# Kernel optimization log

Measured on AMD Instinct MI355X. Metric: run time of the kernel, lower is better.

## Reference

```python
import jax, jax.numpy as jnp
import numpy as np

N, E = 40000, 640000
IN_DIM, EDGE_DIM, HID = 128, 64, 128


def setup_inputs() -> dict:
    key = jax.random.key(0)
    ks = jax.random.split(key, 10)
    x = jax.random.normal(ks[0], (N, IN_DIM), dtype=jnp.float32)
    edge_index = jax.random.randint(ks[1], (2, E), 0, N, dtype=jnp.int64)
    edge_attr = jax.random.normal(ks[2], (E, EDGE_DIM), dtype=jnp.float32)
    # learned params (xavier-ish scaling)
    Wh_w = jax.random.normal(ks[3], (EDGE_DIM, HID), dtype=jnp.float32) / np.sqrt(EDGE_DIM)
    Wh_b = jnp.zeros((HID,), dtype=jnp.float32)
    Wn_w = jax.random.normal(ks[4], (2 * IN_DIM, HID), dtype=jnp.float32) / np.sqrt(2 * IN_DIM)
    Wn_b = jnp.zeros((HID,), dtype=jnp.float32)
    w_e = jax.random.normal(ks[5], (HID, 1), dtype=jnp.float32) / np.sqrt(HID)
    ft_w = jax.random.normal(ks[6], (IN_DIM, IN_DIM), dtype=jnp.float32) / np.sqrt(IN_DIM)
    ft_b = jnp.zeros((IN_DIM,), dtype=jnp.float32)
    return {"x": x, "edge_index": edge_index, "edge_attr": edge_attr,
            "Wh_w": Wh_w, "Wh_b": Wh_b, "Wn_w": Wn_w, "Wn_b": Wn_b,
            "w_e": w_e, "ft_w": ft_w, "ft_b": ft_b}


def reference(x, edge_index, edge_attr, Wh_w, Wh_b, Wn_w, Wn_b, w_e, ft_w, ft_b):
    src, dst = edge_index[0], edge_index[1]
    # gather endpoint features and run edge MLP: relu(W_h(e) + W_n([x_src; x_dst]))
    node_feat = jnp.concatenate([x[src], x[dst]], axis=1)          # [E, 2*in_dim]
    edge_h = edge_attr @ Wh_w + Wh_b                               # [E, hid]
    node_h = node_feat @ Wn_w + Wn_b                               # [E, hid]
    combined = jax.nn.relu(edge_h + node_h)
    scores = (combined @ w_e)[:, 0]                                # [E]
    alpha = jax.nn.softmax(scores, axis=0)                         # softmax over all edges
    # scatter-add weighted dst features into src nodes (same-type branch)
    local = jnp.zeros_like(x).at[src].add(-alpha[:, None] * x[dst])
    out = x + local
    out = out + out @ ft_w + ft_b
    return out
```

## Files before the change

kernel.cpp:

```cpp
#include <hip/hip_runtime.h>
#include <math.h>

#define N_NODES 40000
#define E_EDGES 640000
#define IN_DIM 128
#define EDGE_DIM 64
#define HID 128
#define EB 10000
#define NPART (EB * 4)

typedef unsigned int u32;
typedef unsigned short u16;
typedef __attribute__((ext_vector_type(4))) float f32x4;
typedef __attribute__((ext_vector_type(8))) short bf16x8;

__device__ __forceinline__ float bf_lo(u32 d) { return __uint_as_float(d << 16); }
__device__ __forceinline__ float bf_hi(u32 d) { return __uint_as_float(d & 0xffff0000u); }
__device__ __forceinline__ u16 f2bf(float f) {
    u32 u = __float_as_uint(f);
    return (u16)((u + 0x7fffu + ((u >> 16) & 1u)) >> 16);
}
__device__ __forceinline__ u32 pack_bf(float lo, float hi) {
    return ((u32)f2bf(hi) << 16) | (u32)f2bf(lo);
}


__global__ __launch_bounds__(256) void k_init(const float* __restrict__ x,
                                              u16* __restrict__ xb,
                                              u32* __restrict__ counts) {
    int i = blockIdx.x * 256 + threadIdx.x;
    xb[i] = f2bf(x[i]);
    if (i < N_NODES) counts[i] = 0;
}

__global__ __launch_bounds__(256) void k_trans(const float* __restrict__ Whw,
                                               const float* __restrict__ Wnw,
                                               const float* __restrict__ ftw,
                                               u16* __restrict__ Whtb,
                                               u16* __restrict__ WnAT,
                                               u16* __restrict__ WnBT,
                                               u16* __restrict__ fttb) {
    int i = blockIdx.x * 256 + threadIdx.x;
    if (i < 8192) {
        int h = i >> 6, k = i & 63;
        Whtb[i] = f2bf(Whw[k * HID + h]);
    } else if (i < 24576) {
        int j = i - 8192, h = j >> 7, k = j & 127;
        WnAT[j] = f2bf(Wnw[k * HID + h]);
    } else if (i < 40960) {
        int j = i - 24576, h = j >> 7, k = j & 127;
        WnBT[j] = f2bf(Wnw[(IN_DIM + k) * HID + h]);
    } else {
        int j = i - 40960, h = j >> 7, k = j & 127;
        fttb[j] = f2bf(ftw[k * IN_DIM + h]);
    }
}

__global__ __launch_bounds__(256) void k_proj(const u16* __restrict__ xb,
                                              const u16* __restrict__ WnAT,
                                              const u16* __restrict__ WnBT,
                                              const float* __restrict__ Whb,
                                              const float* __restrict__ Wnb,
                                              u16* __restrict__ P1b,
                                              u16* __restrict__ P2b) {
    const int t = threadIdx.x, w = t >> 6, lane = t & 63;
    const int mrow = lane & 15, quad = lane >> 4;
    const int rowBase = blockIdx.x * 64 + w * 16;

    bf16x8 a[4];
    const u16* ar = xb + (size_t)(rowBase + mrow) * IN_DIM + quad * 8;
#pragma unroll
    for (int ks = 0; ks < 4; ++ks) a[ks] = *(const bf16x8*)(ar + ks * 32);

#pragma unroll
    for (int nt = 0; nt < 8; ++nt) {
        const u16* b1p = WnAT + (size_t)(nt * 16 + mrow) * IN_DIM + quad * 8;
        const u16* b2p = WnBT + (size_t)(nt * 16 + mrow) * IN_DIM + quad * 8;
        f32x4 c1 = {0.f, 0.f, 0.f, 0.f}, c2 = {0.f, 0.f, 0.f, 0.f};
#pragma unroll
        for (int ks = 0; ks < 4; ++ks) {
            c1 = __builtin_amdgcn_mfma_f32_16x16x32_bf16(a[ks], *(const bf16x8*)(b1p + ks * 32), c1, 0, 0, 0);
            c2 = __builtin_amdgcn_mfma_f32_16x16x32_bf16(a[ks], *(const bf16x8*)(b2p + ks * 32), c2, 0, 0, 0);
        }
        const int col = nt * 16 + mrow;
        const float bias = Whb[col] + Wnb[col];
#pragma unroll
        for (int r = 0; r < 4; ++r) {
            int row = rowBase + quad * 4 + r;
            P1b[(size_t)row * HID + col] = f2bf(c1[r] + bias);
            P2b[(size_t)row * HID + col] = f2bf(c2[r]);
        }
    }
}

__global__ __launch_bounds__(256) void k_hist(const int* __restrict__ eidx,
                                              u32* __restrict__ counts) {
    int e = blockIdx.x * 256 + threadIdx.x;
    atomicAdd(&counts[eidx[e]], 1u);
}

__global__ __launch_bounds__(1024) void k_scan(const u32* __restrict__ counts,
                                               u32* __restrict__ off,
                                               u32* __restrict__ cur) {
    __shared__ u32 sums[1024];
    const int t = threadIdx.x;
    const int CH = 40;
    u32 local[CH];
    u32 s = 0;
    const int base = t * CH;
#pragma unroll
    for (int i = 0; i < CH; ++i) {
        int idx = base + i;
        u32 c = (idx < N_NODES) ? counts[idx] : 0u;
        local[i] = s;
        s += c;
    }
    sums[t] = s;
    __syncthreads();
    for (int o = 1; o < 1024; o <<= 1) {
        u32 v = (t >= o) ? sums[t - o] : 0u;
        __syncthreads();
        sums[t] += v;
        __syncthreads();
    }
    const u32 pre = sums[t] - s;
#pragma unroll
    for (int i = 0; i < CH; ++i) {
        int idx = base + i;
        if (idx < N_NODES) {
            u32 v = pre + local[i];
            off[idx] = v;
            cur[idx] = v;
        }
    }
    if (t == 1023) off[N_NODES] = sums[1023];
}

__global__ __launch_bounds__(256) void k_fill(const int* __restrict__ eidx,
                                              u32* __restrict__ cur,
                                              uint2* __restrict__ perm2) {
    int e = blockIdx.x * 256 + threadIdx.x;
    int s = eidx[e];
    int d = eidx[E_EDGES + e];
    u32 pos = atomicAdd(&cur[s], 1u);
    perm2[pos] = make_uint2((u32)e, (u32)d);
}

__global__ __launch_bounds__(256) void k_edge(const int* __restrict__ eidx,
                                              const float* __restrict__ ea,
                                              const u16* __restrict__ Whtb,
                                              const u16* __restrict__ P1b,
                                              const u16* __restrict__ P2b,
                                              const float* __restrict__ we,
                                              const uint2* __restrict__ perm2,
                                              uint2* __restrict__ sde,
                                              float* __restrict__ partials) {
    const int t = threadIdx.x, w = t >> 6, lane = t & 63;
    const int j0 = blockIdx.x * 64 + w * 16;
    const int mrow = lane & 15, quad = lane >> 4;

    const uint2 pe = perm2[j0 + mrow];
    const int em   = (int)pe.x;
    const int dstm = (int)pe.y;
    const int srcm = eidx[em];

    const u16* p1 = P1b + (size_t)srcm * HID + quad * 8;
    const u16* p2 = P2b + (size_t)dstm * HID + quad * 8;
    bf16x8 aP1[4], aP2[4];
#pragma unroll
    for (int ks = 0; ks < 4; ++ks) {
        aP1[ks] = *(const bf16x8*)(p1 + ks * 32);
        aP2[ks] = *(const bf16x8*)(p2 + ks * 32);
    }

    const float* arow = ea + (size_t)em * EDGE_DIM + quad * 8;
    float4 f0 = *(const float4*)(arow);
    float4 f1 = *(const float4*)(arow + 4);
    float4 f2 = *(const float4*)(arow + 32);
    float4 f3 = *(const float4*)(arow + 36);

    bf16x8 bIe, bIo;
    {
        const int hotj = mrow & 7;
        const bool ce = (quad == (mrow >> 3));
        const bool co = (quad == 2 + (mrow >> 3));
#pragma unroll
        for (int j = 0; j < 8; ++j) {
            bIe[j] = (short)((ce && j == hotj) ? 0x3F80 : 0);
            bIo[j] = (short)((co && j == hotj) ? 0x3F80 : 0);
        }
    }

    bf16x8 a0, a1;
    a0[0] = (short)f2bf(f0.x); a0[1] = (short)f2bf(f0.y);
    a0[2] = (short)f2bf(f0.z); a0[3] = (short)f2bf(f0.w);
    a0[4] = (short)f2bf(f1.x); a0[5] = (short)f2bf(f1.y);
    a0[6] = (short)f2bf(f1.z); a0[7] = (short)f2bf(f1.w);
    a1[0] = (short)f2bf(f2.x); a1[1] = (short)f2bf(f2.y);
    a1[2] = (short)f2bf(f2.z); a1[3] = (short)f2bf(f2.w);
    a1[4] = (short)f2bf(f3.x); a1[5] = (short)f2bf(f3.y);
    a1[6] = (short)f2bf(f3.z); a1[7] = (short)f2bf(f3.w);

    float wsum[4] = {0.f, 0.f, 0.f, 0.f};
    const u16* bbase = Whtb + (size_t)mrow * EDGE_DIM + quad * 8;
#pragma unroll
    for (int nt = 0; nt < 8; ++nt) {
        const u16* bp = bbase + nt * 16 * EDGE_DIM;
        bf16x8 b0 = *(const bf16x8*)(bp);
        bf16x8 b1 = *(const bf16x8*)(bp + 32);
        f32x4 c = {0.f, 0.f, 0.f, 0.f};
        c = __builtin_amdgcn_mfma_f32_16x16x32_bf16(a0, b0, c, 0, 0, 0);
        c = __builtin_amdgcn_mfma_f32_16x16x32_bf16(a1, b1, c, 0, 0, 0);
        const bf16x8 bI = (nt & 1) ? bIo : bIe;
        c = __builtin_amdgcn_mfma_f32_16x16x32_bf16(aP1[nt >> 1], bI, c, 0, 0, 0);
        c = __builtin_amdgcn_mfma_f32_16x16x32_bf16(aP2[nt >> 1], bI, c, 0, 0, 0);
        float wv = we[nt * 16 + mrow];
#pragma unroll
        for (int r = 0; r < 4; ++r)
            wsum[r] += fmaxf(c[r], 0.f) * wv;
    }

#pragma unroll
    for (int off = 1; off < 16; off <<= 1) {
#pragma unroll
        for (int r = 0; r < 4; ++r) wsum[r] += __shfl_xor(wsum[r], off, 16);
    }
    float ex[4]; float s4 = 0.f;
#pragma unroll
    for (int r = 0; r < 4; ++r) { ex[r] = __expf(wsum[r]); s4 += ex[r]; }

    u32 dArr[4];
#pragma unroll
    for (int r = 0; r < 4; ++r)
        dArr[r] = (u32)__shfl(dstm, quad * 4 + r, 16);

    if (mrow == 0) {
#pragma unroll
        for (int r = 0; r < 4; ++r)
            sde[j0 + quad * 4 + r] = make_uint2(dArr[r], __float_as_uint(-ex[r]));
    }

    s4 += __shfl_xor(s4, 16, 64);
    s4 += __shfl_xor(s4, 32, 64);
    if (lane == 0) partials[blockIdx.x * 4 + w] = s4;
}

__global__ __launch_bounds__(256) void k_sum(const float* __restrict__ partials,
                                             float* __restrict__ sumExp) {
    float s = 0.f;
    for (int i = threadIdx.x; i < NPART; i += 256) s += partials[i];
#pragma unroll
    for (int off = 1; off < 64; off <<= 1) s += __shfl_xor(s, off, 64);
    __shared__ float ws4[4];
    if ((threadIdx.x & 63) == 0) ws4[threadIdx.x >> 6] = s;
    __syncthreads();
    if (threadIdx.x == 0) sumExp[0] = ws4[0] + ws4[1] + ws4[2] + ws4[3];
}

__global__ __launch_bounds__(256) void k_accum(const u32* __restrict__ off,
                                               const uint2* __restrict__ sde,
                                               const float* __restrict__ sumExp,
                                               const u16* __restrict__ xb,
                                               float* __restrict__ out) {
    const float invS = 1.0f / sumExp[0];
    const int lane = threadIdx.x & 63;
    const int n = blockIdx.x * 4 + (threadIdx.x >> 6);
    const u32 o0 = off[n], o1 = off[n + 1];

    float acc0 = 0.f, acc1 = 0.f;
    for (u32 base = o0; base < o1; base += 64) {
        u32 j = base + (u32)lane;
        uint2 dv = make_uint2(0u, 0u);
        if (j < o1) dv = sde[j];
        int cnt = (int)min(64u, o1 - base);
        int jj = 0;
        for (; jj + 4 <= cnt; jj += 4) {
            u32 d0 = __shfl(dv.x, jj, 64),     d1 = __shfl(dv.x, jj + 1, 64);
            u32 d2 = __shfl(dv.x, jj + 2, 64), d3 = __shfl(dv.x, jj + 3, 64);
            float a0 = __uint_as_float(__shfl(dv.y, jj, 64));
            float a1 = __uint_as_float(__shfl(dv.y, jj + 1, 64));
            float a2 = __uint_as_float(__shfl(dv.y, jj + 2, 64));
            float a3 = __uint_as_float(__shfl(dv.y, jj + 3, 64));
            u32 q0 = ((const u32*)(xb + (size_t)d0 * IN_DIM))[lane];
            u32 q1 = ((const u32*)(xb + (size_t)d1 * IN_DIM))[lane];
            u32 q2 = ((const u32*)(xb + (size_t)d2 * IN_DIM))[lane];
            u32 q3 = ((const u32*)(xb + (size_t)d3 * IN_DIM))[lane];
            acc0 = fmaf(a0, bf_lo(q0), acc0); acc1 = fmaf(a0, bf_hi(q0), acc1);
            acc0 = fmaf(a1, bf_lo(q1), acc0); acc1 = fmaf(a1, bf_hi(q1), acc1);
            acc0 = fmaf(a2, bf_lo(q2), acc0); acc1 = fmaf(a2, bf_hi(q2), acc1);
            acc0 = fmaf(a3, bf_lo(q3), acc0); acc1 = fmaf(a3, bf_hi(q3), acc1);
        }
        for (; jj < cnt; ++jj) {
            u32 dst = __shfl(dv.x, jj, 64);
            float a = __uint_as_float(__shfl(dv.y, jj, 64));
            u32 q = ((const u32*)(xb + (size_t)dst * IN_DIM))[lane];
            acc0 = fmaf(a, bf_lo(q), acc0);
            acc1 = fmaf(a, bf_hi(q), acc1);
        }
    }
    float* op = out + (size_t)n * IN_DIM + 2 * lane;
    op[0] = acc0 * invS;
    op[1] = acc1 * invS;
}

__global__ __launch_bounds__(256) void k_final(const float* __restrict__ x,
                                               const u16* __restrict__ fttb,
                                               const float* __restrict__ ftb,
                                               float* __restrict__ out) {
    __shared__ u32 ybp[64][68];
    const int t = threadIdx.x;
    const int rb = blockIdx.x * 64;

    {
        const int rr = t >> 2, seg = t & 3;
        const float4* xp = (const float4*)(x + (size_t)(rb + rr) * IN_DIM + seg * 32);
        const float4* lp = (const float4*)(out + (size_t)(rb + rr) * IN_DIM + seg * 32);
#pragma unroll
        for (int i = 0; i < 4; ++i) {
            float4 xa = xp[2 * i], xc = xp[2 * i + 1];
            float4 la = lp[2 * i], lc = lp[2 * i + 1];
            uint4 o;
            o.x = pack_bf(xa.x + la.x, xa.y + la.y);
            o.y = pack_bf(xa.z + la.z, xa.w + la.w);
            o.z = pack_bf(xc.x + lc.x, xc.y + lc.y);
            o.w = pack_bf(xc.z + lc.z, xc.w + lc.w);
            *(uint4*)&ybp[rr][seg * 16 + i * 4] = o;
        }
    }
    __syncthreads();

    const int w = t >> 6, lane = t & 63;
    const int mrow = lane & 15, quad = lane >> 4;
    const int rowBase = rb + w * 16;

    bf16x8 a[4];
#pragma unroll
    for (int ks = 0; ks < 4; ++ks)
        a[ks] = *(const bf16x8*)&ybp[w * 16 + mrow][ks * 16 + quad * 4];

#pragma unroll
    for (int nt = 0; nt < 8; ++nt) {
        const u16* bp = fttb + (size_t)(nt * 16 + mrow) * IN_DIM + quad * 8;
        f32x4 c = {0.f, 0.f, 0.f, 0.f};
#pragma unroll
        for (int ks = 0; ks < 4; ++ks)
            c = __builtin_amdgcn_mfma_f32_16x16x32_bf16(a[ks], *(const bf16x8*)(bp + ks * 32), c, 0, 0, 0);
        const int col = nt * 16 + mrow;
        const float fb = ftb[col];
#pragma unroll
        for (int r = 0; r < 4; ++r) {
            int row = rowBase + quad * 4 + r;
            size_t idx = (size_t)row * IN_DIM + col;
            float y = x[idx] + out[idx];
            out[idx] = y + c[r] + fb;
        }
    }
}

extern "C" void kernel_launch(void* const* d_in, const int* in_sizes, int n_in,
                              void* d_out, int out_size, void* d_ws, size_t ws_size,
                              hipStream_t stream) {
    const float* x    = (const float*)d_in[0];
    const int*   eidx = (const int*)d_in[1];
    const float* ea   = (const float*)d_in[2];
    const float* Whw  = (const float*)d_in[3];
    const float* Whb  = (const float*)d_in[4];
    const float* Wnw  = (const float*)d_in[5];
    const float* Wnb  = (const float*)d_in[6];
    const float* we   = (const float*)d_in[7];
    const float* ftw  = (const float*)d_in[8];
    const float* ftb  = (const float*)d_in[9];
    float* out = (float*)d_out;

    uint2* sde      = (uint2*)d_ws;
    u16*   P1b      = (u16*)(sde + (size_t)E_EDGES);
    u16*   P2b      = P1b + (size_t)N_NODES * HID;
    u16*   xb       = P2b + (size_t)N_NODES * HID;
    u16*   Whtb     = xb + (size_t)N_NODES * IN_DIM;
    u16*   WnAT     = Whtb + (size_t)EDGE_DIM * HID;
    u16*   WnBT     = WnAT + (size_t)HID * IN_DIM;
    u16*   fttb     = WnBT + (size_t)HID * IN_DIM;
    float* partials = (float*)(fttb + (size_t)IN_DIM * IN_DIM);
    float* sumExp   = partials + NPART;
    u32*   counts   = (u32*)(sumExp + 1);
    u32*   off      = counts + N_NODES;
    u32*   cur      = off + N_NODES + 1;
    uint2* perm2    = (uint2*)(cur + N_NODES);

    k_init <<<(N_NODES * IN_DIM) / 256, 256, 0, stream>>>(x, xb, counts);
    k_trans<<<224, 256, 0, stream>>>(Whw, Wnw, ftw, Whtb, WnAT, WnBT, fttb);
    k_proj <<<N_NODES / 64, 256, 0, stream>>>(xb, WnAT, WnBT, Whb, Wnb, P1b, P2b);
    k_hist <<<E_EDGES / 256, 256, 0, stream>>>(eidx, counts);
    k_scan <<<1, 1024, 0, stream>>>(counts, off, cur);
    k_fill <<<E_EDGES / 256, 256, 0, stream>>>(eidx, cur, perm2);
    k_edge <<<EB, 256, 0, stream>>>(eidx, ea, Whtb, P1b, P2b, we, perm2, sde, partials);
    k_sum  <<<1, 256, 0, stream>>>(partials, sumExp);
    k_accum<<<N_NODES / 4, 256, 0, stream>>>(off, sde, sumExp, xb, out);
    k_final<<<N_NODES / 64, 256, 0, stream>>>(x, fttb, ftb, out);
}
```

Baseline: 595.5 us.

## Fuse edge scoring with per-node scatter accumulation, defer softmax normalization to final

The edge-score kernel becomes node-centric: each wavefront handles one source node's CSR segment, computes scores for 16 edges at a time and directly accumulates the exp-weighted dst features into the output row. This removes the sde intermediate buffer and the separate k_accum kernel, and the division by the global exp sum moves into k_final. The P1 fragment is loaded once per node instead of once per edge. In exchange, load balance now follows node degree, and partial 16-edge tiles compute padded work.

```diff
diff --git a/kernel.cpp b/kernel.cpp
--- a/kernel.cpp
+++ b/kernel.cpp
@@ -6,8 +6,7 @@
 #define IN_DIM 128
 #define EDGE_DIM 64
 #define HID 128
-#define EB 10000
-#define NPART (EB * 4)
+#define NPART N_NODES
 
 typedef unsigned int u32;
 typedef unsigned short u16;
@@ -146,38 +145,21 @@
     perm2[pos] = make_uint2((u32)e, (u32)d);
 }
 
-__global__ __launch_bounds__(256) void k_edge(const int* __restrict__ eidx,
-                                              const float* __restrict__ ea,
+__global__ __launch_bounds__(256) void k_edge(const float* __restrict__ ea,
                                               const u16* __restrict__ Whtb,
                                               const u16* __restrict__ P1b,
                                               const u16* __restrict__ P2b,
                                               const float* __restrict__ we,
+                                              const u32* __restrict__ off,
                                               const uint2* __restrict__ perm2,
-                                              uint2* __restrict__ sde,
+                                              const u16* __restrict__ xb,
+                                              float* __restrict__ out,
                                               float* __restrict__ partials) {
     const int t = threadIdx.x, w = t >> 6, lane = t & 63;
-    const int j0 = blockIdx.x * 64 + w * 16;
+    const int n = blockIdx.x * 4 + w;
     const int mrow = lane & 15, quad = lane >> 4;
-
-    const uint2 pe = perm2[j0 + mrow];
-    const int em   = (int)pe.x;
-    const int dstm = (int)pe.y;
-    const int srcm = eidx[em];
-
-    const u16* p1 = P1b + (size_t)srcm * HID + quad * 8;
-    const u16* p2 = P2b + (size_t)dstm * HID + quad * 8;
-    bf16x8 aP1[4], aP2[4];
-#pragma unroll
-    for (int ks = 0; ks < 4; ++ks) {
-        aP1[ks] = *(const bf16x8*)(p1 + ks * 32);
-        aP2[ks] = *(const bf16x8*)(p2 + ks * 32);
-    }
-
-    const float* arow = ea + (size_t)em * EDGE_DIM + quad * 8;
-    float4 f0 = *(const float4*)(arow);
-    float4 f1 = *(const float4*)(arow + 4);
-    float4 f2 = *(const float4*)(arow + 32);
-    float4 f3 = *(const float4*)(arow + 36);
+    const u32 o0 = off[n], o1 = off[n + 1];
+    const int deg = (int)(o1 - o0);
 
     bf16x8 bIe, bIo;
     {
@@ -191,58 +173,108 @@
         }
     }
 
-    bf16x8 a0, a1;
-    a0[0] = (short)f2bf(f0.x); a0[1] = (short)f2bf(f0.y);
-    a0[2] = (short)f2bf(f0.z); a0[3] = (short)f2bf(f0.w);
-    a0[4] = (short)f2bf(f1.x); a0[5] = (short)f2bf(f1.y);
-    a0[6] = (short)f2bf(f1.z); a0[7] = (short)f2bf(f1.w);
-    a1[0] = (short)f2bf(f2.x); a1[1] = (short)f2bf(f2.y);
-    a1[2] = (short)f2bf(f2.z); a1[3] = (short)f2bf(f2.w);
-    a1[4] = (short)f2bf(f3.x); a1[5] = (short)f2bf(f3.y);
-    a1[6] = (short)f2bf(f3.z); a1[7] = (short)f2bf(f3.w);
-
-    float wsum[4] = {0.f, 0.f, 0.f, 0.f};
-    const u16* bbase = Whtb + (size_t)mrow * EDGE_DIM + quad * 8;
-#pragma unroll
-    for (int nt = 0; nt < 8; ++nt) {
-        const u16* bp = bbase + nt * 16 * EDGE_DIM;
-        bf16x8 b0 = *(const bf16x8*)(bp);
-        bf16x8 b1 = *(const bf16x8*)(bp + 32);
-        f32x4 c = {0.f, 0.f, 0.f, 0.f};
-        c = __builtin_amdgcn_mfma_f32_16x16x32_bf16(a0, b0, c, 0, 0, 0);
-        c = __builtin_amdgcn_mfma_f32_16x16x32_bf16(a1, b1, c, 0, 0, 0);
-        const bf16x8 bI = (nt & 1) ? bIo : bIe;
-        c = __builtin_amdgcn_mfma_f32_16x16x32_bf16(aP1[nt >> 1], bI, c, 0, 0, 0);
-        c = __builtin_amdgcn_mfma_f32_16x16x32_bf16(aP2[nt >> 1], bI, c, 0, 0, 0);
-        float wv = we[nt * 16 + mrow];
-#pragma unroll
-        for (int r = 0; r < 4; ++r)
-            wsum[r] += fmaxf(c[r], 0.f) * wv;
-    }
-
-#pragma unroll
-    for (int off = 1; off < 16; off <<= 1) {
-#pragma unroll
-        for (int r = 0; r < 4; ++r) wsum[r] += __shfl_xor(wsum[r], off, 16);
-    }
-    float ex[4]; float s4 = 0.f;
-#pragma unroll
-    for (int r = 0; r < 4; ++r) { ex[r] = __expf(wsum[r]); s4 += ex[r]; }
-
-    u32 dArr[4];
-#pragma unroll
-    for (int r = 0; r < 4; ++r)
-        dArr[r] = (u32)__shfl(dstm, quad * 4 + r, 16);
-
-    if (mrow == 0) {
-#pragma unroll
-        for (int r = 0; r < 4; ++r)
-            sde[j0 + quad * 4 + r] = make_uint2(dArr[r], __float_as_uint(-ex[r]));
-    }
+    bf16x8 aP1[4];
+    {
+        const u16* p1 = P1b + (size_t)n * HID + quad * 8;
+#pragma unroll
+        for (int ks = 0; ks < 4; ++ks) aP1[ks] = *(const bf16x8*)(p1 + ks * 32);
+    }
+
+    float wv[8];
+#pragma unroll
+    for (int nt = 0; nt < 8; ++nt) wv[nt] = we[nt * 16 + mrow];
+
+    float acc0 = 0.f, acc1 = 0.f;
+    float s4 = 0.f;
+
+    for (int b0 = 0; b0 < deg; b0 += 16) {
+        const u32 slot = min(o0 + (u32)(b0 + mrow), (u32)(E_EDGES - 1));
+        const uint2 pe = perm2[slot];
+        const int em   = (int)pe.x;
+        const int dstm = (int)pe.y;
+
+        const u16* p2 = P2b + (size_t)dstm * HID + quad * 8;
+        bf16x8 aP2[4];
+#pragma unroll
+        for (int ks = 0; ks < 4; ++ks) aP2[ks] = *(const bf16x8*)(p2 + ks * 32);
+
+        const float* arow = ea + (size_t)em * EDGE_DIM + quad * 8;
+        float4 f0 = *(const float4*)(arow);
+        float4 f1 = *(const float4*)(arow + 4);
+        float4 f2 = *(const float4*)(arow + 32);
+        float4 f3 = *(const float4*)(arow + 36);
+
+        bf16x8 a0, a1;
+        a0[0] = (short)f2bf(f0.x); a0[1] = (short)f2bf(f0.y);
+        a0[2] = (short)f2bf(f0.z); a0[3] = (short)f2bf(f0.w);
+        a0[4] = (short)f2bf(f1.x); a0[5] = (short)f2bf(f1.y);
+        a0[6] = (short)f2bf(f1.z); a0[7] = (short)f2bf(f1.w);
+        a1[0] = (short)f2bf(f2.x); a1[1] = (short)f2bf(f2.y);
+        a1[2] = (short)f2bf(f2.z); a1[3] = (short)f2bf(f2.w);
+        a1[4] = (short)f2bf(f3.x); a1[5] = (short)f2bf(f3.y);
+        a1[6] = (short)f2bf(f3.z); a1[7] = (short)f2bf(f3.w);
+
+        float wsum[4] = {0.f, 0.f, 0.f, 0.f};
+        const u16* bbase = Whtb + (size_t)mrow * EDGE_DIM + quad * 8;
+#pragma unroll
+        for (int nt = 0; nt < 8; ++nt) {
+            const u16* bp = bbase + nt * 16 * EDGE_DIM;
+            bf16x8 b0v = *(const bf16x8*)(bp);
+            bf16x8 b1v = *(const bf16x8*)(bp + 32);
+            f32x4 c = {0.f, 0.f, 0.f, 0.f};
+            c = __builtin_amdgcn_mfma_f32_16x16x32_bf16(a0, b0v, c, 0, 0, 0);
+            c = __builtin_amdgcn_mfma_f32_16x16x32_bf16(a1, b1v, c, 0, 0, 0);
+            const bf16x8 bI = (nt & 1) ? bIo : bIe;
+            c = __builtin_amdgcn_mfma_f32_16x16x32_bf16(aP2[nt >> 1], bI, c, 0, 0, 0);
+            c = __builtin_amdgcn_mfma_f32_16x16x32_bf16(aP1[nt >> 1], bI, c, 0, 0, 0);
+#pragma unroll
+            for (int r = 0; r < 4; ++r)
+                wsum[r] += fmaxf(c[r], 0.f) * wv[nt];
+        }
+
+#pragma unroll
+        for (int o = 1; o < 16; o <<= 1) {
+#pragma unroll
+            for (int r = 0; r < 4; ++r) wsum[r] += __shfl_xor(wsum[r], o, 16);
+        }
+
+        float ex[4];
+#pragma unroll
+        for (int r = 0; r < 4; ++r) {
+            int sl = b0 + quad * 4 + r;
+            ex[r] = (sl < deg) ? __expf(wsum[r]) : 0.f;
+            s4 += ex[r];
+        }
+
+#pragma unroll
+        for (int j = 0; j < 16; j += 4) {
+            const int srcl = (j >> 2) * 16;
+            u32 d0 = (u32)__shfl(dstm, j + 0, 16);
+            u32 d1 = (u32)__shfl(dstm, j + 1, 16);
+            u32 d2 = (u32)__shfl(dstm, j + 2, 16);
+            u32 d3 = (u32)__shfl(dstm, j + 3, 16);
+            float a0v = -__shfl(ex[0], srcl, 64);
+            float a1v = -__shfl(ex[1], srcl, 64);
+            float a2v = -__shfl(ex[2], srcl, 64);
+            float a3v = -__shfl(ex[3], srcl, 64);
+            u32 q0 = ((const u32*)(xb + (size_t)d0 * IN_DIM))[lane];
+            u32 q1 = ((const u32*)(xb + (size_t)d1 * IN_DIM))[lane];
+            u32 q2 = ((const u32*)(xb + (size_t)d2 * IN_DIM))[lane];
+            u32 q3 = ((const u32*)(xb + (size_t)d3 * IN_DIM))[lane];
+            acc0 = fmaf(a0v, bf_lo(q0), acc0); acc1 = fmaf(a0v, bf_hi(q0), acc1);
+            acc0 = fmaf(a1v, bf_lo(q1), acc0); acc1 = fmaf(a1v, bf_hi(q1), acc1);
+            acc0 = fmaf(a2v, bf_lo(q2), acc0); acc1 = fmaf(a2v, bf_hi(q2), acc1);
+            acc0 = fmaf(a3v, bf_lo(q3), acc0); acc1 = fmaf(a3v, bf_hi(q3), acc1);
+        }
+    }
+
+    float* op = out + (size_t)n * IN_DIM + 2 * lane;
+    op[0] = acc0;
+    op[1] = acc1;
 
     s4 += __shfl_xor(s4, 16, 64);
     s4 += __shfl_xor(s4, 32, 64);
-    if (lane == 0) partials[blockIdx.x * 4 + w] = s4;
+    if (lane == 0) partials[n] = s4;
 }
 
 __global__ __launch_bounds__(256) void k_sum(const float* __restrict__ partials,
@@ -257,57 +289,13 @@
     if (threadIdx.x == 0) sumExp[0] = ws4[0] + ws4[1] + ws4[2] + ws4[3];
 }
 
-__global__ __launch_bounds__(256) void k_accum(const u32* __restrict__ off,
-                                               const uint2* __restrict__ sde,
-                                               const float* __restrict__ sumExp,
-                                               const u16* __restrict__ xb,
-                                               float* __restrict__ out) {
-    const float invS = 1.0f / sumExp[0];
-    const int lane = threadIdx.x & 63;
-    const int n = blockIdx.x * 4 + (threadIdx.x >> 6);
-    const u32 o0 = off[n], o1 = off[n + 1];
-
-    float acc0 = 0.f, acc1 = 0.f;
-    for (u32 base = o0; base < o1; base += 64) {
-        u32 j = base + (u32)lane;
-        uint2 dv = make_uint2(0u, 0u);
-        if (j < o1) dv = sde[j];
-        int cnt = (int)min(64u, o1 - base);
-        int jj = 0;
-        for (; jj + 4 <= cnt; jj += 4) {
-            u32 d0 = __shfl(dv.x, jj, 64),     d1 = __shfl(dv.x, jj + 1, 64);
-            u32 d2 = __shfl(dv.x, jj + 2, 64), d3 = __shfl(dv.x, jj + 3, 64);
-            float a0 = __uint_as_float(__shfl(dv.y, jj, 64));
-            float a1 = __uint_as_float(__shfl(dv.y, jj + 1, 64));
-            float a2 = __uint_as_float(__shfl(dv.y, jj + 2, 64));
-            float a3 = __uint_as_float(__shfl(dv.y, jj + 3, 64));
-            u32 q0 = ((const u32*)(xb + (size_t)d0 * IN_DIM))[lane];
-            u32 q1 = ((const u32*)(xb + (size_t)d1 * IN_DIM))[lane];
-            u32 q2 = ((const u32*)(xb + (size_t)d2 * IN_DIM))[lane];
-            u32 q3 = ((const u32*)(xb + (size_t)d3 * IN_DIM))[lane];
-            acc0 = fmaf(a0, bf_lo(q0), acc0); acc1 = fmaf(a0, bf_hi(q0), acc1);
-            acc0 = fmaf(a1, bf_lo(q1), acc0); acc1 = fmaf(a1, bf_hi(q1), acc1);
-            acc0 = fmaf(a2, bf_lo(q2), acc0); acc1 = fmaf(a2, bf_hi(q2), acc1);
-            acc0 = fmaf(a3, bf_lo(q3), acc0); acc1 = fmaf(a3, bf_hi(q3), acc1);
-        }
-        for (; jj < cnt; ++jj) {
-            u32 dst = __shfl(dv.x, jj, 64);
-            float a = __uint_as_float(__shfl(dv.y, jj, 64));
-            u32 q = ((const u32*)(xb + (size_t)dst * IN_DIM))[lane];
-            acc0 = fmaf(a, bf_lo(q), acc0);
-            acc1 = fmaf(a, bf_hi(q), acc1);
-        }
-    }
-    float* op = out + (size_t)n * IN_DIM + 2 * lane;
-    op[0] = acc0 * invS;
-    op[1] = acc1 * invS;
-}
-
 __global__ __launch_bounds__(256) void k_final(const float* __restrict__ x,
                                                const u16* __restrict__ fttb,
                                                const float* __restrict__ ftb,
+                                               const float* __restrict__ sumExp,
                                                float* __restrict__ out) {
     __shared__ u32 ybp[64][68];
+    const float invS = 1.0f / sumExp[0];
     const int t = threadIdx.x;
     const int rb = blockIdx.x * 64;
 
@@ -320,10 +308,10 @@
             float4 xa = xp[2 * i], xc = xp[2 * i + 1];
             float4 la = lp[2 * i], lc = lp[2 * i + 1];
             uint4 o;
-            o.x = pack_bf(xa.x + la.x, xa.y + la.y);
-            o.y = pack_bf(xa.z + la.z, xa.w + la.w);
-            o.z = pack_bf(xc.x + lc.x, xc.y + lc.y);
-            o.w = pack_bf(xc.z + lc.z, xc.w + lc.w);
+            o.x = pack_bf(fmaf(invS, la.x, xa.x), fmaf(invS, la.y, xa.y));
+            o.y = pack_bf(fmaf(invS, la.z, xa.z), fmaf(invS, la.w, xa.w));
+            o.z = pack_bf(fmaf(invS, lc.x, xc.x), fmaf(invS, lc.y, xc.y));
+            o.w = pack_bf(fmaf(invS, lc.z, xc.z), fmaf(invS, lc.w, xc.w));
             *(uint4*)&ybp[rr][seg * 16 + i * 4] = o;
         }
     }
@@ -351,7 +339,7 @@
         for (int r = 0; r < 4; ++r) {
             int row = rowBase + quad * 4 + r;
             size_t idx = (size_t)row * IN_DIM + col;
-            float y = x[idx] + out[idx];
+            float y = fmaf(invS, out[idx], x[idx]);
             out[idx] = y + c[r] + fb;
         }
     }
@@ -372,8 +360,8 @@
     const float* ftb  = (const float*)d_in[9];
     float* out = (float*)d_out;
 
-    uint2* sde      = (uint2*)d_ws;
-    u16*   P1b      = (u16*)(sde + (size_t)E_EDGES);
+    uint2* perm2    = (uint2*)d_ws;
+    u16*   P1b      = (u16*)(perm2 + (size_t)E_EDGES);
     u16*   P2b      = P1b + (size_t)N_NODES * HID;
     u16*   xb       = P2b + (size_t)N_NODES * HID;
     u16*   Whtb     = xb + (size_t)N_NODES * IN_DIM;
@@ -385,7 +373,6 @@
     u32*   counts   = (u32*)(sumExp + 1);
     u32*   off      = counts + N_NODES;
     u32*   cur      = off + N_NODES + 1;
-    uint2* perm2    = (uint2*)(cur + N_NODES);
 
     k_init <<<(N_NODES * IN_DIM) / 256, 256, 0, stream>>>(x, xb, counts);
     k_trans<<<224, 256, 0, stream>>>(Whw, Wnw, ftw, Whtb, WnAT, WnBT, fttb);
@@ -393,8 +380,7 @@
     k_hist <<<E_EDGES / 256, 256, 0, stream>>>(eidx, counts);
     k_scan <<<1, 1024, 0, stream>>>(counts, off, cur);
     k_fill <<<E_EDGES / 256, 256, 0, stream>>>(eidx, cur, perm2);
-    k_edge <<<EB, 256, 0, stream>>>(eidx, ea, Whtb, P1b, P2b, we, perm2, sde, partials);
+    k_edge <<<N_NODES / 4, 256, 0, stream>>>(ea, Whtb, P1b, P2b, we, off, perm2, xb, out, partials);
     k_sum  <<<1, 256, 0, stream>>>(partials, sumExp);
-    k_accum<<<N_NODES / 4, 256, 0, stream>>>(off, sde, sumExp, xb, out);
-    k_final<<<N_NODES / 64, 256, 0, stream>>>(x, fttb, ftb, out);
-}
+    k_final<<<N_NODES / 64, 256, 0, stream>>>(x, fttb, ftb, sumExp, out);
+}
```

Measured after the change: 641.7 us. 7.8% more time.
